# Kernel tuning notes

Hardware: AMD Instinct MI355X
Metric: run time of the kernel (lower is better)

## Reference

```python
import jax, jax.numpy as jnp
import numpy as np

B, L, C, H, V = 64, 512, 256, 4, 32000
D = C // H
DIL = (1, 2, 4)
WIN = 3
NC = (50, 20)
NEG = -1e9


def setup_inputs() -> dict:
    key = jax.random.key(0)
    ks = jax.random.split(key, 20)
    g = lambda i, shape: jax.random.normal(ks[i], shape, jnp.float32) * 0.05
    Lay = len(DIL)
    x = jax.random.randint(ks[0], (B, L), 0, V)
    emb = g(1, (V, C)).at[0].set(0.0)  # padding_idx=0 row is zero
    return dict(
        x=x, emb=emb, pos=g(2, (L, C)),
        gp_W=g(3, (Lay, C, C)), gp_as=g(4, (Lay, H, D)), gp_ad=g(5, (Lay, H, D)),
        gf_W=g(6, (Lay, C, C)), gf_as=g(7, (Lay, H, D)), gf_ad=g(8, (Lay, H, D)),
        msg_W=g(9, (Lay, C, 2 * C)), msg_b=jnp.zeros((Lay, C), jnp.float32),
        gru_Wih=g(10, (Lay, 3 * C, C)), gru_bih=jnp.zeros((Lay, 3 * C), jnp.float32),
        gru_Whh=g(11, (Lay, 3 * C, C)), gru_bhh=jnp.zeros((Lay, 3 * C), jnp.float32),
        ln_g=jnp.ones((Lay, C), jnp.float32), ln_b=jnp.zeros((Lay, C), jnp.float32),
        pool_w=g(12, (C,)), pool_b=jnp.zeros((), jnp.float32),
        h0_W=g(13, (NC[0], C)), h0_b=jnp.zeros((NC[0],), jnp.float32),
        h1_W=g(14, (NC[1], C)), h1_b=jnp.zeros((NC[1],), jnp.float32),
    )


def _dense_gat(x, W, a_src, a_dst, adj):
    # x: [B,L,C], W: [C_out,C_in], a_*: [H,D], adj: [B,L,L] bool
    b, l, _ = x.shape
    h = jnp.einsum('blc,oc->blo', x, W).reshape(b, l, H, D).transpose(0, 2, 1, 3)  # [B,H,L,D]
    s = jnp.einsum('bhld,hd->bhl', h, a_src)
    d = jnp.einsum('bhld,hd->bhl', h, a_dst)
    e = s[:, :, :, None] + d[:, :, None, :]            # [B,H,L,L]
    e = jnp.where(e > 0, e, 0.2 * e)                   # LeakyReLU(0.2)
    e = jnp.where(adj[:, None, :, :], e, NEG)
    alpha = jax.nn.softmax(e, axis=-1)                 # dropout is identity in eval
    out = jnp.einsum('bhij,bhjd->bhid', alpha, h)
    return out.transpose(0, 2, 1, 3).reshape(b, l, C)


def _forward(x, emb, pos, gp_W, gp_as, gp_ad, gf_W, gf_as, gf_ad,
             msg_W, msg_b, gru_Wih, gru_bih, gru_Whh, gru_bhh,
             ln_g, ln_b, pool_w, pool_b, h0_W, h0_b, h1_W, h1_b):
    mask = x != 0                                      # [B,L]
    mf = mask.astype(jnp.float32)[..., None]           # [B,L,1]
    h = (emb[x] + pos[None, :, :] * mf) * mf
    logical = jnp.clip(jnp.cumsum(mask.astype(jnp.int32), axis=1) - 1, 0)
    valid = mask[:, None, :] & mask[:, :, None]        # [B,L,L]
    eye = jnp.eye(L, dtype=bool)[None]
    for l in range(len(DIL)):
        dil = DIL[l]
        diff = logical[:, :, None] - logical[:, None, :]
        ad = jnp.abs(diff)
        in_win = (ad <= WIN * dil) & (ad % dil == 0)
        adj_p = (valid & in_win & (diff < 0)) | eye
        adj_f = (valid & in_win & (diff > 0)) | eye
        m_p = _dense_gat(h, gp_W[l], gp_as[l], gp_ad[l], adj_p)
        m_f = _dense_gat(h, gf_W[l], gf_as[l], gf_ad[l], adj_f)
        m = jnp.concatenate([m_p, m_f], axis=-1)
        m = jax.nn.relu(jnp.einsum('blk,ck->blc', m, msg_W[l]) + msg_b[l])
        # GRUCell(input=m, hidden=h), PyTorch gate order: r,z,n
        gi = jnp.einsum('blc,gc->blg', m, gru_Wih[l]) + gru_bih[l]
        gh = jnp.einsum('blc,gc->blg', h, gru_Whh[l]) + gru_bhh[l]
        ir, iz, inn = jnp.split(gi, 3, axis=-1)
        hr, hz, hn = jnp.split(gh, 3, axis=-1)
        r = jax.nn.sigmoid(ir + hr)
        z = jax.nn.sigmoid(iz + hz)
        n = jnp.tanh(inn + r * hn)
        h_new = (1.0 - z) * n + z * h
        mu = jnp.mean(h_new, axis=-1, keepdims=True)
        var = jnp.mean(jnp.square(h_new - mu), axis=-1, keepdims=True)
        h_new = (h_new - mu) * jax.lax.rsqrt(var + 1e-5) * ln_g[l] + ln_b[l]
        h = h_new * mf
    # attention pooling over sequence (masked softmax on linear scores)
    sc = jnp.einsum('blc,c->bl', h, pool_w) + pool_b
    sc = jnp.where(mask, sc, NEG)
    a = jax.nn.softmax(sc, axis=-1)
    pooled = jnp.einsum('bl,blc->bc', a, h)            # dropout identity in eval
    o0 = pooled @ h0_W.T + h0_b
    o1 = pooled @ h1_W.T + h1_b
    return jnp.concatenate([o0, o1], axis=-1)          # [B, 50+20]


def reference(x, emb, pos, gp_W, gp_as, gp_ad, gf_W, gf_as, gf_ad,
              msg_W, msg_b, gru_Wih, gru_bih, gru_Whh, gru_bhh,
              ln_g, ln_b, pool_w, pool_b, h0_W, h0_b, h1_W, h1_b):
    return _forward(x, emb, pos, gp_W, gp_as, gp_ad, gf_W, gf_as, gf_ad,
                    msg_W, msg_b, gru_Wih, gru_bih, gru_Whh, gru_bhh,
                    ln_g, ln_b, pool_w, pool_b, h0_W, h0_b, h1_W, h1_b)
```

## Files before the change

kernel.cpp:

```cpp
#include <hip/hip_runtime.h>
#include <math.h>

#define B_ 64
#define L_ 512
#define C_ 256
#define H_ 4
#define LAY 3
#define NEGV -1e9f

typedef __attribute__((ext_vector_type(8))) short short8;
typedef __attribute__((ext_vector_type(4))) short short4v;
typedef __attribute__((ext_vector_type(4))) float floatx4;

static __device__ __forceinline__ float rcp_(float x) { return __builtin_amdgcn_rcpf(x); }
static __device__ __forceinline__ float sig_(float x) { return rcp_(1.f + __expf(-x)); }
static __device__ __forceinline__ float tanh_(float x) {
    float e = __expf(2.f * x);
    return 1.f - 2.f * rcp_(e + 1.f);
}

static __device__ __forceinline__ short f2bf(float f) {
    unsigned x = __float_as_uint(f);
    x += 0x7fffu + ((x >> 16) & 1u);
    return (short)(x >> 16);
}
static __device__ __forceinline__ float bf2f(short s) {
    return __uint_as_float(((unsigned)(unsigned short)s) << 16);
}

static __device__ __forceinline__ int tok_swizzle(int blk) {
    int c8 = blk & 7, i = blk >> 3;
    return (c8 + 8 * (i >> 5)) * 128 + (i & 31) * 4;
}

static __device__ __forceinline__ void gl_lds16(const short* g, short* l) {
    __builtin_amdgcn_global_load_lds(
        (const __attribute__((address_space(1))) unsigned int*)g,
        (__attribute__((address_space(3))) unsigned int*)l, 16, 0, 0);
}

#define CF() asm volatile("" ::: "memory")

__global__ void scan_kernel(const int* __restrict__ x, int* __restrict__ mask,
                            int* __restrict__ logical, int* __restrict__ pol,
                            int* __restrict__ nvalid) {
    int b = blockIdx.x, t = threadIdx.x;
    __shared__ int s[L_];
    int m = (x[b * L_ + t] != 0) ? 1 : 0;
    s[t] = m;
    __syncthreads();
    for (int off = 1; off < L_; off <<= 1) {
        int v = (t >= off) ? s[t - off] : 0;
        __syncthreads();
        s[t] += v;
        __syncthreads();
    }
    int cum = s[t];
    int lg = cum - 1; if (lg < 0) lg = 0;
    mask[b * L_ + t] = m;
    logical[b * L_ + t] = lg;
    if (m) pol[b * L_ + lg] = t;
    if (t == L_ - 1) nvalid[b] = cum;
}

__global__ void embed_kernel(const int* __restrict__ x, const float* __restrict__ emb,
                             const float* __restrict__ pos, short* __restrict__ hb) {
    int t = threadIdx.x;
    int bl = tok_swizzle(blockIdx.x) + (t >> 6);
    int lane = t & 63;
    int xv = x[bl];
    float mf = (xv != 0) ? 1.f : 0.f;
    int l = bl & (L_ - 1);
    float4 e = *(const float4*)&emb[(size_t)xv * C_ + lane * 4];
    float4 p = *(const float4*)&pos[(size_t)l * C_ + lane * 4];
    short4v hv4;
    hv4.x = f2bf((e.x + p.x * mf) * mf);
    hv4.y = f2bf((e.y + p.y * mf) * mf);
    hv4.z = f2bf((e.z + p.z * mf) * mf);
    hv4.w = f2bf((e.w + p.w * mf) * mf);
    *(short4v*)&hb[(size_t)bl * C_ + lane * 4] = hv4;
}

__global__ void f2bf_kernel(const float* __restrict__ s, short* __restrict__ d, int n) {
    int i = blockIdx.x * 256 + threadIdx.x;
    if (i < n) d[i] = f2bf(s[i]);
}

__global__ void prep_wcomb(const float* __restrict__ gpW, const float* __restrict__ gfW,
                           const float* __restrict__ gpas, const float* __restrict__ gpad,
                           const float* __restrict__ gfas, const float* __restrict__ gfad,
                           short* __restrict__ Wc) {
    int i = blockIdx.x * 256 + threadIdx.x;
    if (i >= 3 * 640 * 256) return;
    int k = i & 255;
    int r = (i >> 8) % 640;
    int l = i / (640 * 256);
    float v = 0.f;
    if (r < 256) {
        v = gpW[((size_t)l * 256 + r) * 256 + k];
    } else if (r < 512) {
        v = gfW[((size_t)l * 256 + (r - 256)) * 256 + k];
    } else {
        int n = r - 512;
        if (n < 16) {
            int type = n >> 3, dir = (n >> 2) & 1, hh = n & 3;
            const float* a = type ? (dir ? gfad : gpad) : (dir ? gfas : gpas);
            const float* W = dir ? gfW : gpW;
            for (int j = 0; j < 64; j++) {
                float av = a[l * 256 + hh * 64 + j];
                float wv = W[((size_t)l * 256 + hh * 64 + j) * 256 + k];
                v = fmaf(av, wv, v);
            }
        }
    }
    Wc[i] = f2bf(v);
}

__global__ void prep_gru_i(const float* __restrict__ Wih, const float* __restrict__ Whh,
                           short* __restrict__ Bc) {
    int i = blockIdx.x * 256 + threadIdx.x;
    if (i >= 3 * 1024 * 512) return;
    int k = i & 511, np = (i >> 9) & 1023, l = i >> 19;
    int ch = np >> 2, g = np & 3;
    float v = 0.f;
    if (g < 2) {
        v = (k < 256) ? Wih[((size_t)l * 768 + g * 256 + ch) * 256 + k]
                      : Whh[((size_t)l * 768 + g * 256 + ch) * 256 + (k - 256)];
    } else if (g == 2) {
        if (k < 256) v = Wih[((size_t)l * 768 + 512 + ch) * 256 + k];
    } else {
        if (k >= 256) v = Whh[((size_t)l * 768 + 512 + ch) * 256 + (k - 256)];
    }
    Bc[i] = f2bf(v);
}

__global__ void prep_bias4(const float* __restrict__ bih, const float* __restrict__ bhh,
                           float* __restrict__ bc) {
    int i = blockIdx.x * 256 + threadIdx.x;
    if (i >= 3 * 1024) return;
    int np = i & 1023, l = i >> 10;
    int ch = np >> 2, g = np & 3;
    float v;
    if (g < 2)       v = bih[l * 768 + g * 256 + ch] + bhh[l * 768 + g * 256 + ch];
    else if (g == 2) v = bih[l * 768 + 512 + ch];
    else             v = bhh[l * 768 + 512 + ch];
    bc[i] = v;
}

__global__ __launch_bounds__(256) void projssd_bgemm(const short* __restrict__ A0,
                                                     const short* __restrict__ Bw,
                                                     short* __restrict__ hpb2,
                                                     float* __restrict__ Ssd) {
    __shared__ short As[128 * 32];
    __shared__ short Bs[128 * 32];
    const int id = blockIdx.x;
    const int j = id >> 3;
    const int cb = j >> 5;
    const int rb = ((id & 7) << 5) + (j & 31);
    const int tid = threadIdx.x;
    const int wave = tid >> 6, lane = tid & 63;
    const int wm = wave >> 1, wn = wave & 1;
    const size_t arow0 = (size_t)rb * 128;
    const short* Bb = Bw + (size_t)cb * 128 * 256;
    floatx4 acc[4][4];
#pragma unroll
    for (int i = 0; i < 4; i++)
#pragma unroll
        for (int jj = 0; jj < 4; jj++) acc[i][jj] = (floatx4)0.f;

    const int srow = lane >> 2;
    const int sq = (lane & 3) * 8;
    const int q = lane >> 4, t16 = lane & 15;

    for (int k0 = 0; k0 < 256; k0 += 32) {
        const short* Abase = A0 + arow0 * 256 + k0;
#pragma unroll
        for (int t = 0; t < 2; ++t) {
            int r = (wave * 2 + t) * 16 + srow;
            gl_lds16(Abase + (size_t)r * 256 + sq, &As[r * 32 + sq]);
            gl_lds16(Bb + (size_t)r * 256 + k0 + sq, &Bs[r * 32 + sq]);
        }
        __syncthreads();
        short8 af[4], bfr[4];
#pragma unroll
        for (int mf = 0; mf < 4; mf++)
            af[mf] = *(const short8*)&As[(wm * 64 + mf * 16 + t16) * 32 + q * 8];
#pragma unroll
        for (int nf = 0; nf < 4; nf++)
            bfr[nf] = *(const short8*)&Bs[(wn * 64 + nf * 16 + t16) * 32 + q * 8];
#pragma unroll
        for (int mf = 0; mf < 4; mf++)
#pragma unroll
            for (int nf = 0; nf < 4; nf++)
                acc[nf][mf] = __builtin_amdgcn_mfma_f32_16x16x32_bf16(
                    bfr[nf], af[mf], acc[nf][mf], 0, 0, 0);
        __syncthreads();
    }

    const int rowbase = rb * 128 + wm * 64;
    if (cb < 4) {
        const int colbase = cb * 128 + wn * 64;
#pragma unroll
        for (int nf = 0; nf < 4; nf++) {
            int col0 = colbase + nf * 16 + q * 4;
#pragma unroll
            for (int mf = 0; mf < 4; mf++) {
                int row = rowbase + mf * 16 + t16;
                short4v pk;
                pk.x = f2bf(acc[nf][mf][0]);
                pk.y = f2bf(acc[nf][mf][1]);
                pk.z = f2bf(acc[nf][mf][2]);
                pk.w = f2bf(acc[nf][mf][3]);
                *(short4v*)&hpb2[(size_t)row * 512 + col0] = pk;
            }
        }
    } else {
        if (wn == 0) {
            int col0 = q * 4;
            if (col0 < 16) {
#pragma unroll
                for (int mf = 0; mf < 4; mf++) {
                    int row = rowbase + mf * 16 + t16;
                    float4 pk = make_float4(acc[0][mf][0], acc[0][mf][1],
                                            acc[0][mf][2], acc[0][mf][3]);
                    *(float4*)&Ssd[(size_t)row * 16 + col0] = pk;
                }
            }
        }
    }
}

static __device__ __forceinline__ short8 lds_rd8(const short* p) {
    return *(const short8*)p;
}

template <int MH>
static __device__ __forceinline__ void ld_af(const short* bufA, int wm, int q, int t16,
                                             short8 af[4][2]) {
#pragma unroll
    for (int mfl = 0; mfl < 4; ++mfl) {
        int row = wm * 128 + (MH * 4 + mfl) * 16 + t16;
#pragma unroll
        for (int ks = 0; ks < 2; ++ks) {
            int cg = (ks * 4 + q) ^ (row & 7);
            af[mfl][ks] = lds_rd8(&bufA[row * 64 + cg * 8]);
        }
    }
}

template <int NH>
static __device__ __forceinline__ void ld_bf(const short* bufB, int wn, int q, int t16,
                                             short8 bf[2][2]) {
#pragma unroll
    for (int nfl = 0; nfl < 2; ++nfl) {
        int row = wn * 64 + (NH * 2 + nfl) * 16 + t16;
#pragma unroll
        for (int ks = 0; ks < 2; ++ks) {
            int cg = (ks * 4 + q) ^ (row & 7);
            bf[nfl][ks] = lds_rd8(&bufB[row * 64 + cg * 8]);
        }
    }
}

static __device__ __forceinline__ void ld_bf32(const short* bufB, int wn, int q, int t16,
                                               short8 bf[2][2]) {
#pragma unroll
    for (int nfl = 0; nfl < 2; ++nfl) {
        int row = wn * 32 + nfl * 16 + t16;
#pragma unroll
        for (int ks = 0; ks < 2; ++ks) {
            int cg = (ks * 4 + q) ^ (row & 7);
            bf[nfl][ks] = lds_rd8(&bufB[row * 64 + cg * 8]);
        }
    }
}

template <int MH, int NH>
static __device__ __forceinline__ void mfma_q(const short8 af[4][2], const short8 bf[2][2],
                                              floatx4 acc[4][8]) {
    __builtin_amdgcn_s_setprio(1);
#pragma unroll
    for (int ks = 0; ks < 2; ++ks)
#pragma unroll
        for (int mfl = 0; mfl < 4; ++mfl)
#pragma unroll
            for (int nfl = 0; nfl < 2; ++nfl)
                acc[NH * 2 + nfl][MH * 4 + mfl] = __builtin_amdgcn_mfma_f32_16x16x32_bf16(
                    bf[nfl][ks], af[mfl][ks], acc[NH * 2 + nfl][MH * 4 + mfl], 0, 0, 0);
    __builtin_amdgcn_s_setprio(0);
}

template <int MH>
static __device__ __forceinline__ void mfma_m(const short8 af[4][2], const short8 bf[2][2],
                                              floatx4 acc[2][8]) {
    __builtin_amdgcn_s_setprio(1);
#pragma unroll
    for (int ks = 0; ks < 2; ++ks)
#pragma unroll
        for (int mfl = 0; mfl < 4; ++mfl)
#pragma unroll
            for (int nfl = 0; nfl < 2; ++nfl)
                acc[nfl][MH * 4 + mfl] = __builtin_amdgcn_mfma_f32_16x16x32_bf16(
                    bf[nfl][ks], af[mfl][ks], acc[nfl][MH * 4 + mfl], 0, 0, 0);
    __builtin_amdgcn_s_setprio(0);
}

__global__ __launch_bounds__(512, 2) void gru_bgemm(const short* __restrict__ mmb,
                                                    const short* __restrict__ hb_in,
                                                    const short* __restrict__ Bw,
                                                    short* __restrict__ hn2b,
                                                    const float* __restrict__ bias4) {
    __shared__ short lds[2][32768];
    const int id = blockIdx.x;
    const int rb = 16 * (id & 7) + (id >> 5);
    const int cb = (id >> 3) & 3;
    const int tid = threadIdx.x;
    const int wave = tid >> 6, lane = tid & 63;
    const int wm = wave >> 2, wn = wave & 3;
    const int q = lane >> 4, t16 = lane & 15;
    const size_t arow0 = (size_t)rb * 256;
    const short* Bb = Bw + (size_t)cb * 256 * 512;
    const int ord0 = (5 + cb) & 7;

    floatx4 acc[4][8];
#pragma unroll
    for (int i = 0; i < 4; i++)
#pragma unroll
        for (int jj = 0; jj < 8; jj++) acc[i][jj] = (floatx4)0.f;

    auto stageA = [&](int i, int Hh) {
        int tt = (ord0 + i) & 7;
        const short* Asrc = (tt < 4) ? (mmb + tt * 64) : (hb_in + (tt - 4) * 64);
        short* bufA = lds[i & 1];
#pragma unroll
        for (int u = 0; u < 2; ++u) {
            int unit = u * 512 + tid;
            int row = Hh * 128 + (unit >> 3);
            int cs = (unit & 7) ^ (row & 7);
            gl_lds16(Asrc + (arow0 + (size_t)row) * 256 + cs * 8,
                     bufA + Hh * 8192 + unit * 8);
        }
    };
    auto stageB = [&](int i, int Hh) {
        int tt = (ord0 + i) & 7;
        short* bufB = lds[i & 1] + 16384;
#pragma unroll
        for (int u = 0; u < 2; ++u) {
            int unit = u * 512 + tid;
            int row = Hh * 128 + (unit >> 3);
            int cs = (unit & 7) ^ (row & 7);
            gl_lds16(Bb + (size_t)row * 512 + tt * 64 + cs * 8,
                     bufB + Hh * 8192 + unit * 8);
        }
    };

    stageA(0, 0); stageA(0, 1); stageB(0, 0); stageB(0, 1);
    stageA(1, 0); stageA(1, 1); stageB(1, 0); stageB(1, 1);
    asm volatile("s_waitcnt vmcnt(8)" ::: "memory");
    CF(); __builtin_amdgcn_s_barrier(); CF();

    short8 af[4][2], b0[2][2], b1[2][2];

#pragma unroll 2
    for (int t = 0; t < 8; ++t) {
        const short* bufA = lds[t & 1];
        const short* bufB = lds[t & 1] + 16384;

        ld_af<0>(bufA, wm, q, t16, af);
        ld_bf<0>(bufB, wn, q, t16, b0);
        CF(); __builtin_amdgcn_s_barrier();
        asm volatile("s_waitcnt lgkmcnt(0)" ::: "memory");
        mfma_q<0, 0>(af, b0, acc);
        CF(); __builtin_amdgcn_s_barrier(); CF();

        ld_bf<1>(bufB, wn, q, t16, b1);
        CF(); __builtin_amdgcn_s_barrier();
        asm volatile("s_waitcnt lgkmcnt(0)" ::: "memory");
        mfma_q<0, 1>(af, b1, acc);
        CF(); __builtin_amdgcn_s_barrier(); CF();

        ld_af<1>(bufA, wm, q, t16, af);
        if (t < 6) { stageB(t + 2, 0); stageB(t + 2, 1); }
        CF(); __builtin_amdgcn_s_barrier();
        asm volatile("s_waitcnt lgkmcnt(0)" ::: "memory");
        mfma_q<1, 1>(af, b1, acc);
        CF(); __builtin_amdgcn_s_barrier(); CF();

        if (t < 6) { stageA(t + 2, 0); stageA(t + 2, 1); }
        CF(); __builtin_amdgcn_s_barrier();
        mfma_q<1, 0>(af, b0, acc);
        if (t < 6)       asm volatile("s_waitcnt vmcnt(8)" ::: "memory");
        else if (t == 6) asm volatile("s_waitcnt vmcnt(0)" ::: "memory");
        CF(); __builtin_amdgcn_s_barrier(); CF();
    }

    const short* hpt = lds[1];
    short* sO = (short*)lds;
#pragma unroll
    for (int nf = 0; nf < 4; nf++) {
        int chl = wn * 16 + nf * 4 + q;
        int col0 = cb * 256 + wn * 64 + nf * 16 + q * 4;
        float4 bv4 = *(const float4*)&bias4[col0];
#pragma unroll
        for (int mf = 0; mf < 8; mf++) {
            int rowl = wm * 128 + mf * 16 + t16;
            float hp = bf2f(hpt[rowl * 64 + (((chl >> 3) ^ (rowl & 7)) << 3) + (chl & 7)]);
            float r = sig_(acc[nf][mf][0] + bv4.x);
            float z = sig_(acc[nf][mf][1] + bv4.y);
            float nv = tanh_((acc[nf][mf][2] + bv4.z) + r * (acc[nf][mf][3] + bv4.w));
            sO[rowl * 72 + chl] = f2bf((1.f - z) * nv + z * hp);
        }
    }
    __syncthreads();
#pragma unroll
    for (int it = 0; it < 4; ++it) {
        int unit = it * 512 + tid;
        int rowl = unit >> 3, ck = unit & 7;
        *(short8*)&hn2b[(arow0 + rowl) * 256 + cb * 64 + ck * 8] =
            *(const short8*)&sO[rowl * 72 + ck * 8];
    }
}

__global__ __launch_bounds__(512, 2) void msg_bgemm(const short* __restrict__ A0,
                                                    const short* __restrict__ Bw,
                                                    short* __restrict__ Cout,
                                                    const float* __restrict__ bias) {
    __shared__ short lds[2][24576];
    const int id = blockIdx.x;
    const int j = id >> 3;
    const int rb = (id & 7) * 16 + (j & 15);
    const int cb = j >> 4;
    const int tid = threadIdx.x;
    const int wave = tid >> 6, lane = tid & 63;
    const int wm = wave >> 2, wn = wave & 3;
    const int q = lane >> 4, t16 = lane & 15;
    const size_t arow0 = (size_t)rb * 256;
    const short* Bb = Bw + (size_t)cb * 128 * 512;

    floatx4 acc[2][8];
#pragma unroll
    for (int i = 0; i < 2; i++)
#pragma unroll
        for (int jj = 0; jj < 8; jj++) acc[i][jj] = (floatx4)0.f;

    auto stageA = [&](int t, int Hh) {
        short* bufA = lds[t & 1];
#pragma unroll
        for (int u = 0; u < 2; ++u) {
            int unit = u * 512 + tid;
            int row = Hh * 128 + (unit >> 3);
            int cs = (unit & 7) ^ (row & 7);
            gl_lds16(A0 + (arow0 + (size_t)row) * 512 + t * 64 + cs * 8,
                     bufA + Hh * 8192 + unit * 8);
        }
    };
    auto stageB = [&](int t) {
        short* bufB = lds[t & 1] + 16384;
#pragma unroll
        for (int u = 0; u < 2; ++u) {
            int unit = u * 512 + tid;
            int row = unit >> 3;
            int cs = (unit & 7) ^ (row & 7);
            gl_lds16(Bb + (size_t)row * 512 + t * 64 + cs * 8, bufB + unit * 8);
        }
    };

    stageA(0, 0); stageA(0, 1); stageB(0); stageB(1);
    asm volatile("s_waitcnt vmcnt(2)" ::: "memory");
    CF(); __builtin_amdgcn_s_barrier(); CF();

    short8 af[4][2], bfr[2][2];

#pragma unroll 2
    for (int t = 0; t < 8; ++t) {
        const short* bufA = lds[t & 1];
        const short* bufB = lds[t & 1] + 16384;

        ld_af<0>(bufA, wm, q, t16, af);
        ld_bf32(bufB, wn, q, t16, bfr);
        if (t < 7) { stageA(t + 1, 0); stageA(t + 1, 1); }
        CF(); __builtin_amdgcn_s_barrier();
        asm volatile("s_waitcnt lgkmcnt(0)" ::: "memory");
        mfma_m<0>(af, bfr, acc);
        CF(); __builtin_amdgcn_s_barrier(); CF();

        ld_af<1>(bufA, wm, q, t16, af);
        if (t < 6) stageB(t + 2);
        CF(); __builtin_amdgcn_s_barrier();
        asm volatile("s_waitcnt lgkmcnt(0)" ::: "memory");
        mfma_m<1>(af, bfr, acc);
        if (t < 6)       asm volatile("s_waitcnt vmcnt(2)" ::: "memory");
        else if (t == 6) asm volatile("s_waitcnt vmcnt(0)" ::: "memory");
        CF(); __builtin_amdgcn_s_barrier(); CF();
    }

    short* sO = (short*)lds;
#pragma unroll
    for (int nf = 0; nf < 2; nf++) {
        int chl = wn * 32 + nf * 16 + q * 4;
        int col0 = cb * 128 + chl;
        float4 bv4 = *(const float4*)&bias[col0];
#pragma unroll
        for (int mf = 0; mf < 8; mf++) {
            int rowl = wm * 128 + mf * 16 + t16;
            short4v pk;
            pk.x = f2bf(fmaxf(acc[nf][mf][0] + bv4.x, 0.f));
            pk.y = f2bf(fmaxf(acc[nf][mf][1] + bv4.y, 0.f));
            pk.z = f2bf(fmaxf(acc[nf][mf][2] + bv4.z, 0.f));
            pk.w = f2bf(fmaxf(acc[nf][mf][3] + bv4.w, 0.f));
            *(short4v*)&sO[rowl * 132 + chl] = pk;
        }
    }
    __syncthreads();
#pragma unroll
    for (int it = 0; it < 8; ++it) {
        int unit = it * 512 + tid;
        int rowl = unit >> 4, ck = unit & 15;
        *(short8*)&Cout[(arow0 + rowl) * 256 + cb * 128 + ck * 8] =
            *(const short8*)&sO[rowl * 132 + ck * 8];
    }
}

__global__ __launch_bounds__(256) void ln_kernel(
    const short* __restrict__ hn2b, short* __restrict__ hb,
    const int* __restrict__ mask,
    const float* __restrict__ lng, const float* __restrict__ lnb) {
    int t = threadIdx.x;
    int bl = tok_swizzle(blockIdx.x) + (t >> 6);
    int lane = t & 63;
    short4v v4 = *(const short4v*)&hn2b[(size_t)bl * C_ + lane * 4];
    float v[4] = {bf2f(v4.x), bf2f(v4.y), bf2f(v4.z), bf2f(v4.w)};
    float s = (v[0] + v[1]) + (v[2] + v[3]);
    float ss = (v[0] * v[0] + v[1] * v[1]) + (v[2] * v[2] + v[3] * v[3]);
#pragma unroll
    for (int off = 32; off; off >>= 1) {
        s += __shfl_xor(s, off);
        ss += __shfl_xor(ss, off);
    }
    float mu = s * (1.f / 256.f);
    float var = ss * (1.f / 256.f) - mu * mu;
    float rstd = rsqrtf(fmaxf(var, 0.f) + 1e-5f);
    float4 lg = *(const float4*)&lng[lane * 4];
    float4 lb = *(const float4*)&lnb[lane * 4];
    float mfv = mask[bl] ? 1.f : 0.f;
    short4v yb;
    yb.x = f2bf(((v[0] - mu) * rstd * lg.x + lb.x) * mfv);
    yb.y = f2bf(((v[1] - mu) * rstd * lg.y + lb.y) * mfv);
    yb.z = f2bf(((v[2] - mu) * rstd * lg.z + lb.z) * mfv);
    yb.w = f2bf(((v[3] - mu) * rstd * lg.w + lb.w) * mfv);
    *(short4v*)&hb[(size_t)bl * C_ + lane * 4] = yb;
}

__global__ __launch_bounds__(256) void agg_fused(
    const short* __restrict__ hpb2, const float* __restrict__ S,
    const int* __restrict__ mask, const int* __restrict__ logical,
    const int* __restrict__ pol, const int* __restrict__ nvalid,
    short* __restrict__ m, int dil) {
    int t = threadIdx.x;
    int bl = tok_swizzle(blockIdx.x) + (t >> 6);
    int sub = t & 63;
    int dir = sub >> 5;
    int slot = sub & 31;
    int cb = slot * 8;
    int head = slot >> 3;
    int b = bl >> 9;

    int mi = mask[bl];
    int li = logical[bl];
    int nv = nvalid[b];
    int js[3]; int nn = 0;
    if (mi) {
#pragma unroll
        for (int k = 1; k <= 3; k++) {
            int lj = dir ? (li - k * dil) : (li + k * dil);
            if (lj >= 0 && lj < nv) js[nn++] = pol[b * L_ + lj];
        }
    }
    int sn = dir * 4 + head, dn = 8 + sn;
    float si = S[(size_t)bl * 16 + sn];
    float di = S[(size_t)bl * 16 + dn];
    float e0 = si + di; e0 = e0 > 0.f ? e0 : 0.2f * e0;
    float emax = e0, ev[3];
    for (int k = 0; k < nn; k++) {
        float djv = S[((size_t)(b * L_ + js[k])) * 16 + dn];
        float e = si + djv; e = e > 0.f ? e : 0.2f * e;
        ev[k] = e; emax = fmaxf(emax, e);
    }
    float w0 = __expf(e0 - emax), den = w0;
    float wv[3];
    for (int k = 0; k < nn; k++) { wv[k] = __expf(ev[k] - emax); den += wv[k]; }
    float rden = rcp_(den);

    size_t base = (size_t)bl * 512 + dir * 256 + cb;
    short8 vself = *(const short8*)&hpb2[base];
    float o[8];
#pragma unroll
    for (int j = 0; j < 8; j++) o[j] = w0 * bf2f(vself[j]);
    for (int k = 0; k < nn; k++) {
        short8 vn = *(const short8*)&hpb2[((size_t)(b * L_ + js[k])) * 512 + dir * 256 + cb];
#pragma unroll
        for (int j = 0; j < 8; j++) o[j] = fmaf(wv[k], bf2f(vn[j]), o[j]);
    }
    short8 ov;
#pragma unroll
    for (int j = 0; j < 8; j++) ov[j] = f2bf(o[j] * rden);
    *(short8*)&m[base] = ov;
}

__global__ __launch_bounds__(1024) void pool_head_kernel(
    const short* __restrict__ hb, const int* __restrict__ mask,
    const float* __restrict__ pw, const float* __restrict__ pb,
    const float* __restrict__ h0W, const float* __restrict__ h0b,
    const float* __restrict__ h1W, const float* __restrict__ h1b,
    float* __restrict__ out) {
    int b = blockIdx.x;
    int t = threadIdx.x;
    int lane = t & 63, wave = t >> 6;
    __shared__ float sc[L_];
    __shared__ float red[20];
    __shared__ float part[4][C_];
    __shared__ float pooled[C_];

    float4 wv = *(const float4*)&pw[lane * 4];
    for (int l = wave; l < L_; l += 16) {
        short4v hv = *(const short4v*)&hb[((size_t)b * L_ + l) * C_ + lane * 4];
        float p = bf2f(hv.x) * wv.x + bf2f(hv.y) * wv.y
                + bf2f(hv.z) * wv.z + bf2f(hv.w) * wv.w;
#pragma unroll
        for (int off = 32; off; off >>= 1) p += __shfl_down(p, off);
        if (lane == 0) sc[l] = mask[b * L_ + l] ? (p + pb[0]) : NEGV;
    }
    __syncthreads();

    float v = (t < L_) ? sc[t] : NEGV;
    float mx = v;
#pragma unroll
    for (int off = 32; off; off >>= 1) mx = fmaxf(mx, __shfl_down(mx, off));
    if (lane == 0) red[wave] = mx;
    __syncthreads();
    if (t == 0) {
        float g = red[0];
        for (int i = 1; i < 16; i++) g = fmaxf(g, red[i]);
        red[16] = g;
    }
    __syncthreads();
    float gmax = red[16];
    float e = (t < L_) ? __expf(v - gmax) : 0.f;
    float ssum = e;
#pragma unroll
    for (int off = 32; off; off >>= 1) ssum += __shfl_down(ssum, off);
    if (lane == 0) red[wave] = ssum;
    __syncthreads();
    if (t == 0) {
        float g = 0.f;
        for (int i = 0; i < 16; i++) g += red[i];
        red[17] = 1.f / g;
    }
    __syncthreads();
    if (t < L_) sc[t] = e * red[17];
    __syncthreads();

    int g = t >> 8, c = t & 255;
    const short* hrow = &hb[((size_t)b * L_ + g * 128) * C_ + c];
    const float* scg = &sc[g * 128];
    float a0 = 0.f, a1 = 0.f, a2 = 0.f, a3 = 0.f;
    for (int l = 0; l < 128; l += 4) {
        a0 = fmaf(scg[l + 0], bf2f(hrow[(size_t)(l + 0) * C_]), a0);
        a1 = fmaf(scg[l + 1], bf2f(hrow[(size_t)(l + 1) * C_]), a1);
        a2 = fmaf(scg[l + 2], bf2f(hrow[(size_t)(l + 2) * C_]), a2);
        a3 = fmaf(scg[l + 3], bf2f(hrow[(size_t)(l + 3) * C_]), a3);
    }
    part[g][c] = (a0 + a1) + (a2 + a3);
    __syncthreads();
    if (t < C_) pooled[t] = (part[0][t] + part[1][t]) + (part[2][t] + part[3][t]);
    __syncthreads();

    for (int o = wave; o < 70; o += 16) {
        const float* W = (o < 50) ? (h0W + (size_t)o * C_) : (h1W + (size_t)(o - 50) * C_);
        float bb = (o < 50) ? h0b[o] : h1b[o - 50];
        float4 w4 = *(const float4*)&W[lane * 4];
        float4 p4 = *(const float4*)&pooled[lane * 4];
        float s = p4.x * w4.x + p4.y * w4.y + p4.z * w4.z + p4.w * w4.w;
#pragma unroll
        for (int off = 32; off; off >>= 1) s += __shfl_down(s, off);
        if (lane == 0) out[b * 70 + o] = s + bb;
    }
}

extern "C" void kernel_launch(void* const* d_in, const int* in_sizes, int n_in,
                              void* d_out, int out_size, void* d_ws, size_t ws_size,
                              hipStream_t stream) {
    const int*   x    = (const int*)d_in[0];
    const float* emb  = (const float*)d_in[1];
    const float* pos  = (const float*)d_in[2];
    const float* gpW  = (const float*)d_in[3];
    const float* gpas = (const float*)d_in[4];
    const float* gpad = (const float*)d_in[5];
    const float* gfW  = (const float*)d_in[6];
    const float* gfas = (const float*)d_in[7];
    const float* gfad = (const float*)d_in[8];
    const float* msgW = (const float*)d_in[9];
    const float* msgb = (const float*)d_in[10];
    const float* Wih  = (const float*)d_in[11];
    const float* bih  = (const float*)d_in[12];
    const float* Whh  = (const float*)d_in[13];
    const float* bhh  = (const float*)d_in[14];
    const float* lng  = (const float*)d_in[15];
    const float* lnb  = (const float*)d_in[16];
    const float* pw   = (const float*)d_in[17];
    const float* pb   = (const float*)d_in[18];
    const float* h0W  = (const float*)d_in[19];
    const float* h0b  = (const float*)d_in[20];
    const float* h1W  = (const float*)d_in[21];
    const float* h1b  = (const float*)d_in[22];
    float* out = (float*)d_out;

    const size_t MW = 1024 * 1024;
    float* ws = (float*)d_ws;
    short* hn2b = (short*)ws;
    short* hb   = (short*)(ws + 8 * MW);
    short* mmb  = (short*)(ws + 12 * MW);
    float* Ssd  = ws + 12 * MW;
    short* hpb2 = (short*)(ws + 16 * MW);
    short* mb   = (short*)(ws + 24 * MW);
    short* Wcomb = (short*)(ws + 32 * MW);
    short* msgWb = Wcomb + 3 * 640 * 256;
    short* Bcat  = msgWb + 3 * 256 * 512;
    float* bias4 = (float*)(Bcat + 3 * 1024 * 512);
    int* mask    = (int*)(bias4 + 3 * 1024);
    int* logical = mask + B_ * L_;
    int* pol     = logical + B_ * L_;
    int* nvalid  = pol + B_ * L_;

    prep_wcomb<<<(3 * 640 * 256 + 255) / 256, 256, 0, stream>>>(gpW, gfW, gpas, gpad,
                                                                gfas, gfad, Wcomb);
    f2bf_kernel<<<(3 * 256 * 512 + 255) / 256, 256, 0, stream>>>(msgW, msgWb, 3 * 256 * 512);
    prep_gru_i<<<(3 * 1024 * 512 + 255) / 256, 256, 0, stream>>>(Wih, Whh, Bcat);
    prep_bias4<<<12, 256, 0, stream>>>(bih, bhh, bias4);

    scan_kernel<<<B_, L_, 0, stream>>>(x, mask, logical, pol, nvalid);
    embed_kernel<<<B_ * L_ / 4, 256, 0, stream>>>(x, emb, pos, hb);

    const int DILS[LAY] = {1, 2, 4};

    for (int l = 0; l < LAY; l++) {
        int dil = DILS[l];
        projssd_bgemm<<<256 * 5, 256, 0, stream>>>(hb, Wcomb + (size_t)l * 640 * 256,
                                                   hpb2, Ssd);
        agg_fused<<<8192, 256, 0, stream>>>(hpb2, Ssd, mask, logical, pol, nvalid, mb, dil);
        msg_bgemm<<<256, 512, 0, stream>>>(mb, msgWb + (size_t)l * 256 * 512,
                                           mmb, msgb + l * C_);
        gru_bgemm<<<512, 512, 0, stream>>>(mmb, hb, Bcat + (size_t)l * 1024 * 512,
                                           hn2b, bias4 + l * 1024);
        ln_kernel<<<8192, 256, 0, stream>>>(hn2b, hb, mask, lng + l * C_, lnb + l * C_);
    }

    pool_head_kernel<<<B_, 1024, 0, stream>>>(hb, mask, pw, pb, h0W, h0b, h1W, h1b, out);
}
```

Measured before the change: 500.5 us.

## Rewrite projection GEMM with larger double-buffered tiles and LDS-staged epilogue

Replaces the 128x128-tile, 256-thread projection GEMM with a 256x128-tile, 512-thread kernel. The new kernel uses swizzled LDS, double-buffered global-to-LDS staging with explicit waitcnt/barrier pipelining, and stages the bf16 output through LDS so global stores are coalesced. This is meant to cut redundant weight loads, hide load latency behind MFMA, and improve store efficiency. It also fully unrolls the GRU GEMM loop and adds sched_barriers, which may raise register pressure or code size.

```diff
diff --git a/kernel.cpp b/kernel.cpp
--- a/kernel.cpp
+++ b/kernel.cpp
@@ -147,162 +147,194 @@
     bc[i] = v;
 }
 
-__global__ __launch_bounds__(256) void projssd_bgemm(const short* __restrict__ A0,
-                                                     const short* __restrict__ Bw,
-                                                     short* __restrict__ hpb2,
-                                                     float* __restrict__ Ssd) {
-    __shared__ short As[128 * 32];
-    __shared__ short Bs[128 * 32];
+static __device__ __forceinline__ short8 lds_rd8(const short* p) {
+    return *(const short8*)p;
+}
+
+template <int MH>
+static __device__ __forceinline__ void ld_af(const short* bufA, int wm, int q, int t16,
+                                             short8 af[4][2]) {
+#pragma unroll
+    for (int mfl = 0; mfl < 4; ++mfl) {
+        int row = wm * 128 + (MH * 4 + mfl) * 16 + t16;
+#pragma unroll
+        for (int ks = 0; ks < 2; ++ks) {
+            int cg = (ks * 4 + q) ^ (row & 7);
+            af[mfl][ks] = lds_rd8(&bufA[row * 64 + cg * 8]);
+        }
+    }
+}
+
+template <int NH>
+static __device__ __forceinline__ void ld_bf(const short* bufB, int wn, int q, int t16,
+                                             short8 bf[2][2]) {
+#pragma unroll
+    for (int nfl = 0; nfl < 2; ++nfl) {
+        int row = wn * 64 + (NH * 2 + nfl) * 16 + t16;
+#pragma unroll
+        for (int ks = 0; ks < 2; ++ks) {
+            int cg = (ks * 4 + q) ^ (row & 7);
+            bf[nfl][ks] = lds_rd8(&bufB[row * 64 + cg * 8]);
+        }
+    }
+}
+
+static __device__ __forceinline__ void ld_bf32(const short* bufB, int wn, int q, int t16,
+                                               short8 bf[2][2]) {
+#pragma unroll
+    for (int nfl = 0; nfl < 2; ++nfl) {
+        int row = wn * 32 + nfl * 16 + t16;
+#pragma unroll
+        for (int ks = 0; ks < 2; ++ks) {
+            int cg = (ks * 4 + q) ^ (row & 7);
+            bf[nfl][ks] = lds_rd8(&bufB[row * 64 + cg * 8]);
+        }
+    }
+}
+
+template <int MH, int NH>
+static __device__ __forceinline__ void mfma_q(const short8 af[4][2], const short8 bf[2][2],
+                                              floatx4 acc[4][8]) {
+    __builtin_amdgcn_s_setprio(1);
+#pragma unroll
+    for (int ks = 0; ks < 2; ++ks)
+#pragma unroll
+        for (int mfl = 0; mfl < 4; ++mfl)
+#pragma unroll
+            for (int nfl = 0; nfl < 2; ++nfl)
+                acc[NH * 2 + nfl][MH * 4 + mfl] = __builtin_amdgcn_mfma_f32_16x16x32_bf16(
+                    bf[nfl][ks], af[mfl][ks], acc[NH * 2 + nfl][MH * 4 + mfl], 0, 0, 0);
+    __builtin_amdgcn_s_setprio(0);
+}
+
+template <int MH>
+static __device__ __forceinline__ void mfma_m(const short8 af[4][2], const short8 bf[2][2],
+                                              floatx4 acc[2][8]) {
+    __builtin_amdgcn_s_setprio(1);
+#pragma unroll
+    for (int ks = 0; ks < 2; ++ks)
+#pragma unroll
+        for (int mfl = 0; mfl < 4; ++mfl)
+#pragma unroll
+            for (int nfl = 0; nfl < 2; ++nfl)
+                acc[nfl][MH * 4 + mfl] = __builtin_amdgcn_mfma_f32_16x16x32_bf16(
+                    bf[nfl][ks], af[mfl][ks], acc[nfl][MH * 4 + mfl], 0, 0, 0);
+    __builtin_amdgcn_s_setprio(0);
+}
+
+__global__ __launch_bounds__(512, 2) void projssd_deep(const short* __restrict__ A0,
+                                                       const short* __restrict__ Bw,
+                                                       short* __restrict__ hpb2,
+                                                       float* __restrict__ Ssd) {
+    __shared__ short lds[2][24576];
     const int id = blockIdx.x;
     const int j = id >> 3;
-    const int cb = j >> 5;
-    const int rb = ((id & 7) << 5) + (j & 31);
+    const int cb = j >> 4;
+    const int rb = (id & 7) * 16 + (j & 15);
     const int tid = threadIdx.x;
     const int wave = tid >> 6, lane = tid & 63;
-    const int wm = wave >> 1, wn = wave & 1;
-    const size_t arow0 = (size_t)rb * 128;
+    const int wm = wave >> 2, wn = wave & 3;
+    const int q = lane >> 4, t16 = lane & 15;
+    const size_t arow0 = (size_t)rb * 256;
     const short* Bb = Bw + (size_t)cb * 128 * 256;
-    floatx4 acc[4][4];
-#pragma unroll
-    for (int i = 0; i < 4; i++)
-#pragma unroll
-        for (int jj = 0; jj < 4; jj++) acc[i][jj] = (floatx4)0.f;
-
-    const int srow = lane >> 2;
-    const int sq = (lane & 3) * 8;
-    const int q = lane >> 4, t16 = lane & 15;
-
-    for (int k0 = 0; k0 < 256; k0 += 32) {
-        const short* Abase = A0 + arow0 * 256 + k0;
-#pragma unroll
-        for (int t = 0; t < 2; ++t) {
-            int r = (wave * 2 + t) * 16 + srow;
-            gl_lds16(Abase + (size_t)r * 256 + sq, &As[r * 32 + sq]);
-            gl_lds16(Bb + (size_t)r * 256 + k0 + sq, &Bs[r * 32 + sq]);
-        }
-        __syncthreads();
-        short8 af[4], bfr[4];
-#pragma unroll
-        for (int mf = 0; mf < 4; mf++)
-            af[mf] = *(const short8*)&As[(wm * 64 + mf * 16 + t16) * 32 + q * 8];
-#pragma unroll
-        for (int nf = 0; nf < 4; nf++)
-            bfr[nf] = *(const short8*)&Bs[(wn * 64 + nf * 16 + t16) * 32 + q * 8];
-#pragma unroll
-        for (int mf = 0; mf < 4; mf++)
-#pragma unroll
-            for (int nf = 0; nf < 4; nf++)
-                acc[nf][mf] = __builtin_amdgcn_mfma_f32_16x16x32_bf16(
-                    bfr[nf], af[mf], acc[nf][mf], 0, 0, 0);
-        __syncthreads();
-    }
-
-    const int rowbase = rb * 128 + wm * 64;
+
+    floatx4 acc[2][8];
+#pragma unroll
+    for (int i = 0; i < 2; i++)
+#pragma unroll
+        for (int jj = 0; jj < 8; jj++) acc[i][jj] = (floatx4)0.f;
+
+    auto stageA = [&](int t, int Hh) {
+        short* bufA = lds[t & 1];
+#pragma unroll
+        for (int u = 0; u < 2; ++u) {
+            int unit = u * 512 + tid;
+            int row = Hh * 128 + (unit >> 3);
+            int cs = (unit & 7) ^ (row & 7);
+            gl_lds16(A0 + (arow0 + (size_t)row) * 256 + t * 64 + cs * 8,
+                     bufA + Hh * 8192 + unit * 8);
+        }
+    };
+    auto stageB = [&](int t) {
+        short* bufB = lds[t & 1] + 16384;
+#pragma unroll
+        for (int u = 0; u < 2; ++u) {
+            int unit = u * 512 + tid;
+            int row = unit >> 3;
+            int cs = (unit & 7) ^ (row & 7);
+            gl_lds16(Bb + (size_t)row * 256 + t * 64 + cs * 8, bufB + unit * 8);
+        }
+    };
+
+    stageA(0, 0); stageA(0, 1); stageB(0); stageB(1);
+    asm volatile("s_waitcnt vmcnt(2)" ::: "memory");
+    CF(); __builtin_amdgcn_s_barrier(); CF();
+
+    short8 af[4][2], bfr[2][2];
+
+#pragma unroll
+    for (int t = 0; t < 4; ++t) {
+        const short* bufA = lds[t & 1];
+        const short* bufB = lds[t & 1] + 16384;
+
+        ld_af<0>(bufA, wm, q, t16, af);
+        ld_bf32(bufB, wn, q, t16, bfr);
+        if (t < 3) { stageA(t + 1, 0); stageA(t + 1, 1); }
+        CF(); __builtin_amdgcn_s_barrier();
+        asm volatile("s_waitcnt lgkmcnt(0)" ::: "memory");
+        __builtin_amdgcn_sched_barrier(0);
+        mfma_m<0>(af, bfr, acc);
+        CF(); __builtin_amdgcn_s_barrier(); CF();
+
+        ld_af<1>(bufA, wm, q, t16, af);
+        if (t < 2) stageB(t + 2);
+        CF(); __builtin_amdgcn_s_barrier();
+        asm volatile("s_waitcnt lgkmcnt(0)" ::: "memory");
+        __builtin_amdgcn_sched_barrier(0);
+        mfma_m<1>(af, bfr, acc);
+        if (t < 2)       asm volatile("s_waitcnt vmcnt(2)" ::: "memory");
+        else if (t == 2) asm volatile("s_waitcnt vmcnt(0)" ::: "memory");
+        CF(); __builtin_amdgcn_s_barrier(); CF();
+    }
+
     if (cb < 4) {
-        const int colbase = cb * 128 + wn * 64;
-#pragma unroll
-        for (int nf = 0; nf < 4; nf++) {
-            int col0 = colbase + nf * 16 + q * 4;
-#pragma unroll
-            for (int mf = 0; mf < 4; mf++) {
-                int row = rowbase + mf * 16 + t16;
+        short* sO = (short*)lds;
+#pragma unroll
+        for (int nf = 0; nf < 2; nf++) {
+            int chl = wn * 32 + nf * 16 + q * 4;
+#pragma unroll
+            for (int mf = 0; mf < 8; mf++) {
+                int rowl = wm * 128 + mf * 16 + t16;
                 short4v pk;
                 pk.x = f2bf(acc[nf][mf][0]);
                 pk.y = f2bf(acc[nf][mf][1]);
                 pk.z = f2bf(acc[nf][mf][2]);
                 pk.w = f2bf(acc[nf][mf][3]);
-                *(short4v*)&hpb2[(size_t)row * 512 + col0] = pk;
+                *(short4v*)&sO[rowl * 132 + chl] = pk;
             }
+        }
+        __syncthreads();
+#pragma unroll
+        for (int it = 0; it < 8; ++it) {
+            int unit = it * 512 + tid;
+            int rowl = unit >> 4, ck = unit & 15;
+            *(short8*)&hpb2[(arow0 + rowl) * 512 + cb * 128 + ck * 8] =
+                *(const short8*)&sO[rowl * 132 + ck * 8];
         }
     } else {
         if (wn == 0) {
-            int col0 = q * 4;
-            if (col0 < 16) {
-#pragma unroll
-                for (int mf = 0; mf < 4; mf++) {
-                    int row = rowbase + mf * 16 + t16;
+            int chl = q * 4;
+            if (chl < 16) {
+#pragma unroll
+                for (int mf = 0; mf < 8; mf++) {
+                    int rowl = wm * 128 + mf * 16 + t16;
                     float4 pk = make_float4(acc[0][mf][0], acc[0][mf][1],
                                             acc[0][mf][2], acc[0][mf][3]);
-                    *(float4*)&Ssd[(size_t)row * 16 + col0] = pk;
+                    *(float4*)&Ssd[(arow0 + rowl) * 16 + chl] = pk;
                 }
             }
         }
     }
-}
-
-static __device__ __forceinline__ short8 lds_rd8(const short* p) {
-    return *(const short8*)p;
-}
-
-template <int MH>
-static __device__ __forceinline__ void ld_af(const short* bufA, int wm, int q, int t16,
-                                             short8 af[4][2]) {
-#pragma unroll
-    for (int mfl = 0; mfl < 4; ++mfl) {
-        int row = wm * 128 + (MH * 4 + mfl) * 16 + t16;
-#pragma unroll
-        for (int ks = 0; ks < 2; ++ks) {
-            int cg = (ks * 4 + q) ^ (row & 7);
-            af[mfl][ks] = lds_rd8(&bufA[row * 64 + cg * 8]);
-        }
-    }
-}
-
-template <int NH>
-static __device__ __forceinline__ void ld_bf(const short* bufB, int wn, int q, int t16,
-                                             short8 bf[2][2]) {
-#pragma unroll
-    for (int nfl = 0; nfl < 2; ++nfl) {
-        int row = wn * 64 + (NH * 2 + nfl) * 16 + t16;
-#pragma unroll
-        for (int ks = 0; ks < 2; ++ks) {
-            int cg = (ks * 4 + q) ^ (row & 7);
-            bf[nfl][ks] = lds_rd8(&bufB[row * 64 + cg * 8]);
-        }
-    }
-}
-
-static __device__ __forceinline__ void ld_bf32(const short* bufB, int wn, int q, int t16,
-                                               short8 bf[2][2]) {
-#pragma unroll
-    for (int nfl = 0; nfl < 2; ++nfl) {
-        int row = wn * 32 + nfl * 16 + t16;
-#pragma unroll
-        for (int ks = 0; ks < 2; ++ks) {
-            int cg = (ks * 4 + q) ^ (row & 7);
-            bf[nfl][ks] = lds_rd8(&bufB[row * 64 + cg * 8]);
-        }
-    }
-}
-
-template <int MH, int NH>
-static __device__ __forceinline__ void mfma_q(const short8 af[4][2], const short8 bf[2][2],
-                                              floatx4 acc[4][8]) {
-    __builtin_amdgcn_s_setprio(1);
-#pragma unroll
-    for (int ks = 0; ks < 2; ++ks)
-#pragma unroll
-        for (int mfl = 0; mfl < 4; ++mfl)
-#pragma unroll
-            for (int nfl = 0; nfl < 2; ++nfl)
-                acc[NH * 2 + nfl][MH * 4 + mfl] = __builtin_amdgcn_mfma_f32_16x16x32_bf16(
-                    bf[nfl][ks], af[mfl][ks], acc[NH * 2 + nfl][MH * 4 + mfl], 0, 0, 0);
-    __builtin_amdgcn_s_setprio(0);
-}
-
-template <int MH>
-static __device__ __forceinline__ void mfma_m(const short8 af[4][2], const short8 bf[2][2],
-                                              floatx4 acc[2][8]) {
-    __builtin_amdgcn_s_setprio(1);
-#pragma unroll
-    for (int ks = 0; ks < 2; ++ks)
-#pragma unroll
-        for (int mfl = 0; mfl < 4; ++mfl)
-#pragma unroll
-            for (int nfl = 0; nfl < 2; ++nfl)
-                acc[nfl][MH * 4 + mfl] = __builtin_amdgcn_mfma_f32_16x16x32_bf16(
-                    bf[nfl][ks], af[mfl][ks], acc[nfl][MH * 4 + mfl], 0, 0, 0);
-    __builtin_amdgcn_s_setprio(0);
 }
 
 __global__ __launch_bounds__(512, 2) void gru_bgemm(const short* __restrict__ mmb,
@@ -361,7 +393,7 @@
 
     short8 af[4][2], b0[2][2], b1[2][2];
 
-#pragma unroll 2
+#pragma unroll
     for (int t = 0; t < 8; ++t) {
         const short* bufA = lds[t & 1];
         const short* bufB = lds[t & 1] + 16384;
@@ -370,12 +402,14 @@
         ld_bf<0>(bufB, wn, q, t16, b0);
         CF(); __builtin_amdgcn_s_barrier();
         asm volatile("s_waitcnt lgkmcnt(0)" ::: "memory");
+        __builtin_amdgcn_sched_barrier(0);
         mfma_q<0, 0>(af, b0, acc);
         CF(); __builtin_amdgcn_s_barrier(); CF();
 
         ld_bf<1>(bufB, wn, q, t16, b1);
         CF(); __builtin_amdgcn_s_barrier();
         asm volatile("s_waitcnt lgkmcnt(0)" ::: "memory");
+        __builtin_amdgcn_sched_barrier(0);
         mfma_q<0, 1>(af, b1, acc);
         CF(); __builtin_amdgcn_s_barrier(); CF();
 
@@ -383,6 +417,7 @@
         if (t < 6) { stageB(t + 2, 0); stageB(t + 2, 1); }
         CF(); __builtin_amdgcn_s_barrier();
         asm volatile("s_waitcnt lgkmcnt(0)" ::: "memory");
+        __builtin_amdgcn_sched_barrier(0);
         mfma_q<1, 1>(af, b1, acc);
         CF(); __builtin_amdgcn_s_barrier(); CF();
 
@@ -745,8 +780,8 @@
 
     for (int l = 0; l < LAY; l++) {
         int dil = DILS[l];
-        projssd_bgemm<<<256 * 5, 256, 0, stream>>>(hb, Wcomb + (size_t)l * 640 * 256,
-                                                   hpb2, Ssd);
+        projssd_deep<<<640, 512, 0, stream>>>(hb, Wcomb + (size_t)l * 640 * 256,
+                                              hpb2, Ssd);
         agg_fused<<<8192, 256, 0, stream>>>(hpb2, Ssd, mask, logical, pol, nvalid, mb, dil);
         msg_bgemm<<<256, 512, 0, stream>>>(mb, msgWb + (size_t)l * 256 * 512,
                                            mmb, msgb + l * C_);
```

After: 492.0 us. Within noise of the previous version (-1.7%).
